# Performance work log

Hardware: AMD Instinct MI355X
Metric: run time of the kernel (lower is better)

Reference implementation:

```python
import jax, jax.numpy as jnp
import numpy as np

N, E, F_IN, HID, HEADS, L, G = 20000, 200000, 20, 128, 4, 4, 32
NEG_SLOPE = 0.2


def setup_inputs() -> dict:
    key = jax.random.key(0)
    ks = jax.random.split(key, 12)
    s = 0.05
    x = jax.random.normal(ks[0], (N, F_IN), jnp.float32)
    edge_index = jax.random.randint(ks[1], (2, E), 0, N, jnp.int32)
    batch = jnp.sort(jax.random.randint(ks[2], (N,), 0, G, jnp.int32))
    W_in = jax.random.normal(ks[3], (F_IN, HID), jnp.float32) * s
    b_in = jnp.zeros((HID,), jnp.float32)
    gat_W = jax.random.normal(ks[4], (L, HID, HEADS * HID), jnp.float32) * s
    att_src = jax.random.normal(ks[5], (L, HEADS, HID), jnp.float32) * s
    att_dst = jax.random.normal(ks[6], (L, HEADS, HID), jnp.float32) * s
    gat_b = jnp.zeros((L, HID), jnp.float32)
    W1 = jax.random.normal(ks[7], (HID, HID // 2), jnp.float32) * s
    b1 = jnp.zeros((HID // 2,), jnp.float32)
    W2 = jax.random.normal(ks[8], (HID // 2, 64), jnp.float32) * s
    b2 = jnp.zeros((64,), jnp.float32)
    W3 = jax.random.normal(ks[9], (64, 32), jnp.float32) * s
    b3 = jnp.zeros((32,), jnp.float32)
    return dict(x=x, edge_index=edge_index, batch=batch, W_in=W_in, b_in=b_in,
                gat_W=gat_W, att_src=att_src, att_dst=att_dst, gat_b=gat_b,
                W1=W1, b1=b1, W2=W2, b2=b2, W3=W3, b3=b3)


def _gat_layer(x, src, dst, W, a_src, a_dst, b):
    # x: [N, HID]; W: [HID, HEADS*HID]; a_*: [HEADS, HID]
    xl = (x @ W).reshape(N, HEADS, HID)                      # [N, H, C]
    al_src = jnp.einsum('nhc,hc->nh', xl, a_src)             # [N, H]
    al_dst = jnp.einsum('nhc,hc->nh', xl, a_dst)             # [N, H]
    e = jax.nn.leaky_relu(al_src[src] + al_dst[dst], NEG_SLOPE)  # [Etot, H]
    # segment softmax over incoming edges of each dst node
    m = jax.ops.segment_max(e, dst, num_segments=N)          # [N, H]
    e = jnp.exp(e - m[dst])
    z = jax.ops.segment_sum(e, dst, num_segments=N)          # [N, H]
    alpha = e / (z[dst] + 1e-16)                             # [Etot, H]
    msg = xl[src] * alpha[:, :, None]                        # [Etot, H, C]
    out = jax.ops.segment_sum(msg, dst, num_segments=N)      # [N, H, C]
    return out.mean(axis=1) + b                              # concat=False: mean over heads


def reference(x, edge_index, batch, W_in, b_in, gat_W, att_src, att_dst, gat_b,
              W1, b1, W2, b2, W3, b3):
    # add self-loops (PyG GATConv default)
    loops = jnp.arange(N, dtype=edge_index.dtype)
    src = jnp.concatenate([edge_index[0], loops])
    dst = jnp.concatenate([edge_index[1], loops])
    h = jax.nn.relu(x @ W_in + b_in)
    for l in range(L):
        h = jax.nn.relu(_gat_layer(h, src, dst, gat_W[l], att_src[l], att_dst[l], gat_b[l])) + h
    # global mean pool per graph
    sums = jax.ops.segment_sum(h, batch, num_segments=G)     # [G, HID]
    cnt = jax.ops.segment_sum(jnp.ones((N,), h.dtype), batch, num_segments=G)
    g = sums / jnp.maximum(cnt, 1.0)[:, None]
    # output MLP (dropout is identity in eval mode)
    g = jax.nn.relu(g @ W1 + b1)
    g = jax.nn.relu(g @ W2 + b2)
    return g @ W3 + b3                                        # [G, 32]
```

## Files before the change

kernel.cpp:

```cpp
#include <hip/hip_runtime.h>

#define N_NODES 20000
#define N_PAD   20032
#define N_EDGES 200000
#define ETOT    (N_EDGES + N_NODES)
#define F_IN    20
#define HID     128
#define HEADS   4
#define FTOT    (HEADS * HID)
#define LAYERS  4
#define NGRAPH  32
#define NEG_SLOPE 0.2f

typedef __attribute__((ext_vector_type(8))) unsigned short ushortx8;
typedef __attribute__((ext_vector_type(8))) short short8;
typedef __attribute__((ext_vector_type(4))) float f32x4;

static __device__ __forceinline__ unsigned short f2bf(float f) {
    unsigned u = __float_as_uint(f);
    u += 0x7FFFu + ((u >> 16) & 1u);
    return (unsigned short)(u >> 16);
}
static __device__ __forceinline__ float bf2f(unsigned short s) {
    return __uint_as_float(((unsigned)s) << 16);
}


__global__ void k_hist(const int* __restrict__ ei, int* __restrict__ deg) {
    int i = blockIdx.x * blockDim.x + threadIdx.x;
    if (i >= ETOT) return;
    int d = (i < N_EDGES) ? ei[N_EDGES + i] : (i - N_EDGES);
    atomicAdd(&deg[d], 1);
}

__global__ __launch_bounds__(1024) void k_scan(const int* __restrict__ deg, int* __restrict__ off) {
    __shared__ int wsum[16];
    __shared__ int carry_s;
    int tid  = threadIdx.x;
    int lane = tid & 63, wv = tid >> 6;
    if (tid == 0) carry_s = 0;
    __syncthreads();
    for (int base = 0; base < N_NODES; base += 1024) {
        int idx = base + tid;
        int v = (idx < N_NODES) ? deg[idx] : 0;
        int x = v;
        #pragma unroll
        for (int s = 1; s < 64; s <<= 1) {
            int t = __shfl_up(x, s, 64);
            if (lane >= s) x += t;
        }
        if (lane == 63) wsum[wv] = x;
        __syncthreads();
        if (wv == 0) {
            int ws = (lane < 16) ? wsum[lane] : 0;
            #pragma unroll
            for (int s = 1; s < 16; s <<= 1) {
                int t = __shfl_up(ws, s, 64);
                if (lane >= s) ws += t;
            }
            if (lane < 16) wsum[lane] = ws;
        }
        __syncthreads();
        int wprev = (wv == 0) ? 0 : wsum[wv - 1];
        int incl  = carry_s + wprev + x;
        if (idx < N_NODES) off[idx] = incl - v;
        __syncthreads();
        if (tid == 1023) carry_s = incl;
        __syncthreads();
    }
    if (threadIdx.x == 0) off[N_NODES] = carry_s;
}

__global__ void k_scatter(const int* __restrict__ ei, const int* __restrict__ off,
                          int* __restrict__ cur, int* __restrict__ csr_src) {
    int i = blockIdx.x * blockDim.x + threadIdx.x;
    if (i >= ETOT) return;
    int s, d;
    if (i < N_EDGES) { s = ei[i]; d = ei[N_EDGES + i]; }
    else             { s = d = i - N_EDGES; }
    int pos = off[d] + atomicAdd(&cur[d], 1);
    csr_src[pos] = s;
}


__global__ void k_bounds(const int* __restrict__ batch, int* __restrict__ gstart) {
    int i = blockIdx.x * blockDim.x + threadIdx.x;
    if (i >= N_NODES) return;
    int b = batch[i];
    int prev = (i == 0) ? -1 : batch[i - 1];
    for (int g = prev + 1; g <= b; ++g) gstart[g] = i;
    if (i == N_NODES - 1) {
        for (int g = b + 1; g <= NGRAPH; ++g) gstart[g] = N_NODES;
    }
}


__global__ void k_wconv(const float* __restrict__ W, unsigned short* __restrict__ wswz) {
    int o = blockIdx.x * 256 + threadIdx.x;
    if (o >= LAYERS * 32 * 4 * 64 * 8) return;
    int e    = o & 7;
    int lane = (o >> 3) & 63;
    int kc   = (o >> 9) & 3;
    int cg   = (o >> 11) & 31;
    int l    = o >> 16;
    int k    = kc * 32 + (lane >> 4) * 8 + e;
    int col  = cg * 16 + (lane & 15);
    wswz[o] = f2bf(W[((size_t)l * HID + k) * FTOT + col]);
}


__global__ __launch_bounds__(256) void k_inproj(const float* __restrict__ x,
                                                const float* __restrict__ W,
                                                const float* __restrict__ b,
                                                float* __restrict__ h,
                                                unsigned short* __restrict__ hb) {
    __shared__ float xs[2][F_IN];
    int tid = threadIdx.x;
    int node0 = blockIdx.x * 2;
    if (tid < 2 * F_IN) {
        int r = tid / F_IN, k = tid % F_IN;
        int nd = node0 + r;
        xs[r][k] = (nd < N_NODES) ? x[nd * F_IN + k] : 0.f;
    }
    __syncthreads();
    int ln = tid >> 7;
    int c  = tid & 127;
    int node = node0 + ln;
    if (node >= N_NODES) return;
    float s = b[c];
    #pragma unroll
    for (int k = 0; k < F_IN; ++k) s += xs[ln][k] * W[k * HID + c];
    float r = fmaxf(s, 0.f);
    h[(size_t)node * HID + c] = r;
    hb[(size_t)node * HID + c] = f2bf(r);
}


__global__ __launch_bounds__(256) void k_gemm(const unsigned short* __restrict__ hb,
                                              const unsigned short* __restrict__ wswz,
                                              unsigned short* __restrict__ xl) {
    int tid  = threadIdx.x;
    int lane = tid & 63;
    int w    = tid >> 6;
    int r0   = blockIdx.x * 64 + w * 16;
    int cgb  = blockIdx.y * 4;
    int arow = r0 + (lane & 15);
    const short8* ap = (const short8*)(hb + (size_t)arow * HID + (lane >> 4) * 8);
    const short8* bp = (const short8*)wswz;
    short8 a[4];
    #pragma unroll
    for (int kc = 0; kc < 4; ++kc) a[kc] = ap[kc * 4];
    f32x4 acc[4];
    #pragma unroll
    for (int ct = 0; ct < 4; ++ct) {
        f32x4 c = {0.f, 0.f, 0.f, 0.f};
        int cg = cgb + ct;
        #pragma unroll
        for (int kc = 0; kc < 4; ++kc) {
            short8 b = bp[(cg * 4 + kc) * 64 + lane];
            c = __builtin_amdgcn_mfma_f32_16x16x32_bf16(a[kc], b, c, 0, 0, 0);
        }
        acc[ct] = c;
    }
    int orow = r0 + (lane >> 4) * 4;
    int ocol = lane & 15;
    #pragma unroll
    for (int ct = 0; ct < 4; ++ct) {
        int col = (cgb + ct) * 16 + ocol;
        #pragma unroll
        for (int r = 0; r < 4; ++r) {
            int row = orow + r;
            if (row < N_NODES) xl[(size_t)row * FTOT + col] = f2bf(acc[ct][r]);
        }
    }
}


__global__ __launch_bounds__(256) void k_att(const unsigned short* __restrict__ xl,
                                             const float* __restrict__ asrc,
                                             const float* __restrict__ adst,
                                             float* __restrict__ al_s,
                                             float* __restrict__ al_d) {
    int wid  = threadIdx.x >> 6;
    int lane = threadIdx.x & 63;
    int node = blockIdx.x * 4 + wid;
    if (node >= N_NODES) return;
    int base = lane * 8;
    ushortx8 xv = *(const ushortx8*)(xl + (size_t)node * FTOT + base);
    float xf[8];
    #pragma unroll
    for (int j = 0; j < 8; ++j) xf[j] = bf2f(xv[j]);
    const float4* s4 = (const float4*)(asrc + base);
    const float4* d4 = (const float4*)(adst + base);
    float4 s0 = s4[0], s1 = s4[1], dd0 = d4[0], dd1 = d4[1];
    float ps = xf[0]*s0.x + xf[1]*s0.y + xf[2]*s0.z + xf[3]*s0.w
             + xf[4]*s1.x + xf[5]*s1.y + xf[6]*s1.z + xf[7]*s1.w;
    float pd = xf[0]*dd0.x + xf[1]*dd0.y + xf[2]*dd0.z + xf[3]*dd0.w
             + xf[4]*dd1.x + xf[5]*dd1.y + xf[6]*dd1.z + xf[7]*dd1.w;
    #pragma unroll
    for (int m = 1; m < 16; m <<= 1) {
        ps += __shfl_xor(ps, m, 64);
        pd += __shfl_xor(pd, m, 64);
    }
    if ((lane & 15) == 0) {
        int hh = lane >> 4;
        al_s[node * HEADS + hh] = ps;
        al_d[node * HEADS + hh] = pd;
    }
}


__global__ __launch_bounds__(256) void k_agg(const unsigned short* __restrict__ xl,
                                             const float* __restrict__ al_s,
                                             const float* __restrict__ al_d,
                                             const int* __restrict__ csr_off,
                                             const int* __restrict__ csr_src,
                                             const float* __restrict__ bias,
                                             float* __restrict__ h,
                                             unsigned short* __restrict__ hb) {
    int wid  = threadIdx.x >> 6;
    int lane = threadIdx.x & 63;
    int node = blockIdx.x * 4 + wid;
    if (node >= N_NODES) return;
    int hh = lane >> 4;
    int e0 = csr_off[node], e1 = csr_off[node + 1];
    float ald = al_d[node * HEADS + hh];

    float m = -1e30f, z = 0.f;
    for (int e = e0 + (lane & 15); e < e1; e += 16) {
        int s = csr_src[e];
        float ev = al_s[s * HEADS + hh] + ald;
        ev = ev > 0.f ? ev : NEG_SLOPE * ev;
        float mn = fmaxf(m, ev);
        z = z * __expf(m - mn) + __expf(ev - mn);
        m = mn;
    }
    #pragma unroll
    for (int msk = 1; msk < 16; msk <<= 1) {
        float m2 = __shfl_xor(m, msk, 64);
        float z2 = __shfl_xor(z, msk, 64);
        float mn = fmaxf(m, m2);
        z = z * __expf(m - mn) + z2 * __expf(m2 - mn);
        m = mn;
    }
    float zinv = 1.f / (z + 1e-16f);

    float acc[8] = {};
    #pragma unroll 2
    for (int e = e0; e < e1; ++e) {
        int s = csr_src[e];
        float ev = al_s[s * HEADS + hh] + ald;
        ev = ev > 0.f ? ev : NEG_SLOPE * ev;
        float alpha = __expf(ev - m) * zinv;
        ushortx8 v = *(const ushortx8*)(xl + (size_t)s * FTOT + lane * 8);
        #pragma unroll
        for (int j = 0; j < 8; ++j) acc[j] += alpha * bf2f(v[j]);
    }
    #pragma unroll
    for (int j = 0; j < 8; ++j) {
        acc[j] += __shfl_xor(acc[j], 16, 64);
        acc[j] += __shfl_xor(acc[j], 32, 64);
    }
    if (lane < 16) {
        int c = lane * 8;
        float4 hv0 = *(const float4*)(h + (size_t)node * HID + c);
        float4 hv1 = *(const float4*)(h + (size_t)node * HID + c + 4);
        float4 b0 = *(const float4*)(bias + c);
        float4 b1 = *(const float4*)(bias + c + 4);
        float4 o0, o1;
        o0.x = fmaxf(acc[0] * 0.25f + b0.x, 0.f) + hv0.x;
        o0.y = fmaxf(acc[1] * 0.25f + b0.y, 0.f) + hv0.y;
        o0.z = fmaxf(acc[2] * 0.25f + b0.z, 0.f) + hv0.z;
        o0.w = fmaxf(acc[3] * 0.25f + b0.w, 0.f) + hv0.w;
        o1.x = fmaxf(acc[4] * 0.25f + b1.x, 0.f) + hv1.x;
        o1.y = fmaxf(acc[5] * 0.25f + b1.y, 0.f) + hv1.y;
        o1.z = fmaxf(acc[6] * 0.25f + b1.z, 0.f) + hv1.z;
        o1.w = fmaxf(acc[7] * 0.25f + b1.w, 0.f) + hv1.w;
        *(float4*)(h + (size_t)node * HID + c)     = o0;
        *(float4*)(h + (size_t)node * HID + c + 4) = o1;
        ushortx8 hv;
        hv[0] = f2bf(o0.x); hv[1] = f2bf(o0.y); hv[2] = f2bf(o0.z); hv[3] = f2bf(o0.w);
        hv[4] = f2bf(o1.x); hv[5] = f2bf(o1.y); hv[6] = f2bf(o1.z); hv[7] = f2bf(o1.w);
        *(ushortx8*)(hb + (size_t)node * HID + c) = hv;
    }
}


__global__ __launch_bounds__(128) void k_pool(const float* __restrict__ h,
                                              const int* __restrict__ gstart,
                                              float* __restrict__ pooled) {
    int g = blockIdx.y;
    int slice = blockIdx.x;
    int tid = threadIdx.x;
    int start = gstart[g];
    int cnt   = gstart[g + 1] - start;
    int per = (cnt + 31) / 32;
    int r0 = slice * per, r1 = min(r0 + per, cnt);
    if (r0 >= r1) return;
    float s0 = 0.f, s1 = 0.f, s2 = 0.f, s3 = 0.f;
    int r = r0;
    for (; r + 3 < r1; r += 4) {
        s0 += h[(size_t)(start + r)     * HID + tid];
        s1 += h[(size_t)(start + r + 1) * HID + tid];
        s2 += h[(size_t)(start + r + 2) * HID + tid];
        s3 += h[(size_t)(start + r + 3) * HID + tid];
    }
    for (; r < r1; ++r) s0 += h[(size_t)(start + r) * HID + tid];
    atomicAdd(&pooled[g * HID + tid], (s0 + s1) + (s2 + s3));
}

__global__ __launch_bounds__(256) void k_mlp(const float* __restrict__ pooled,
                                             const int* __restrict__ gstart,
                                             const float* __restrict__ W1, const float* __restrict__ b1,
                                             const float* __restrict__ W2, const float* __restrict__ b2,
                                             const float* __restrict__ W3, const float* __restrict__ b3,
                                             float* __restrict__ out) {
    int gr = blockIdx.x;
    __shared__ float g[HID];
    __shared__ float part[4][64];
    __shared__ float t1[64], t2[64];
    int tid = threadIdx.x;
    if (tid < HID) {
        float inv = 1.f / fmaxf((float)(gstart[gr + 1] - gstart[gr]), 1.f);
        g[tid] = pooled[gr * HID + tid] * inv;
    }
    __syncthreads();
    {
        int c = tid & 63, q = tid >> 6;
        float s = 0.f;
        #pragma unroll 8
        for (int k = q * 32; k < q * 32 + 32; ++k) s += g[k] * W1[k * 64 + c];
        part[q][c] = s;
        __syncthreads();
        if (tid < 64) t1[tid] = fmaxf(part[0][tid] + part[1][tid] + part[2][tid] + part[3][tid] + b1[tid], 0.f);
        __syncthreads();
    }
    {
        int c = tid & 63, q = tid >> 6;
        float s = 0.f;
        #pragma unroll 8
        for (int k = q * 16; k < q * 16 + 16; ++k) s += t1[k] * W2[k * 64 + c];
        part[q][c] = s;
        __syncthreads();
        if (tid < 64) t2[tid] = fmaxf(part[0][tid] + part[1][tid] + part[2][tid] + part[3][tid] + b2[tid], 0.f);
        __syncthreads();
    }
    {
        int c = tid & 31, q = tid >> 5;
        float s = 0.f;
        #pragma unroll 8
        for (int k = q * 8; k < q * 8 + 8; ++k) s += t2[k] * W3[k * 32 + c];
        float* pf = &part[0][0];
        pf[q * 32 + c] = s;
        __syncthreads();
        if (tid < 32) {
            float r = b3[tid];
            #pragma unroll
            for (int q2 = 0; q2 < 8; ++q2) r += pf[q2 * 32 + tid];
            out[gr * 32 + tid] = r;
        }
    }
}


extern "C" void kernel_launch(void* const* d_in, const int* in_sizes, int n_in,
                              void* d_out, int out_size, void* d_ws, size_t ws_size,
                              hipStream_t stream) {
    const float* x       = (const float*)d_in[0];
    const int*   ei      = (const int*)d_in[1];
    const int*   batch   = (const int*)d_in[2];
    const float* W_in    = (const float*)d_in[3];
    const float* b_in    = (const float*)d_in[4];
    const float* gat_W   = (const float*)d_in[5];
    const float* att_src = (const float*)d_in[6];
    const float* att_dst = (const float*)d_in[7];
    const float* gat_b   = (const float*)d_in[8];
    const float* W1 = (const float*)d_in[9];
    const float* b1 = (const float*)d_in[10];
    const float* W2 = (const float*)d_in[11];
    const float* b2 = (const float*)d_in[12];
    const float* W3 = (const float*)d_in[13];
    const float* b3 = (const float*)d_in[14];
    float* out = (float*)d_out;

    char* ws = (char*)d_ws;
    size_t o = 0;
    auto alloc = [&](size_t nbytes) -> void* {
        void* p = ws + o;
        o += (nbytes + 255) & ~(size_t)255;
        return p;
    };
    int* deg      = (int*)alloc((size_t)2 * N_NODES * 4);
    int* cur      = deg + N_NODES;
    int* gstart   = (int*)alloc((size_t)(NGRAPH + 1) * 4);
    float* pooled = (float*)alloc((size_t)NGRAPH * HID * 4);
    int* csr_off  = (int*)alloc((size_t)(N_NODES + 1) * 4);
    int* csr_src  = (int*)alloc((size_t)ETOT * 4);
    float* h      = (float*)alloc((size_t)N_NODES * HID * 4);
    unsigned short* hb   = (unsigned short*)alloc((size_t)N_PAD * HID * 2);
    unsigned short* xl   = (unsigned short*)alloc((size_t)N_NODES * FTOT * 2);
    unsigned short* wswz = (unsigned short*)alloc((size_t)LAYERS * HID * FTOT * 2);
    float* al_s   = (float*)alloc((size_t)N_NODES * HEADS * 4);
    float* al_d   = (float*)alloc((size_t)N_NODES * HEADS * 4);

    hipMemsetAsync(deg, 0, (size_t)2 * N_NODES * 4, stream);
    hipMemsetAsync(pooled, 0, (size_t)NGRAPH * HID * 4, stream);

    k_hist<<<(ETOT + 255) / 256, 256, 0, stream>>>(ei, deg);
    k_scan<<<1, 1024, 0, stream>>>(deg, csr_off);
    k_scatter<<<(ETOT + 255) / 256, 256, 0, stream>>>(ei, csr_off, cur, csr_src);
    k_bounds<<<(N_NODES + 255) / 256, 256, 0, stream>>>(batch, gstart);
    k_wconv<<<(LAYERS * 32 * 4 * 64 * 8) / 256, 256, 0, stream>>>(gat_W, wswz);

    k_inproj<<<(N_NODES + 1) / 2, 256, 0, stream>>>(x, W_in, b_in, h, hb);

    for (int l = 0; l < LAYERS; ++l) {
        k_gemm<<<dim3(N_PAD / 64, FTOT / 64), 256, 0, stream>>>(
            hb, wswz + (size_t)l * HID * FTOT, xl);
        k_att<<<(N_NODES + 3) / 4, 256, 0, stream>>>(
            xl, att_src + (size_t)l * HEADS * HID, att_dst + (size_t)l * HEADS * HID, al_s, al_d);
        k_agg<<<(N_NODES + 3) / 4, 256, 0, stream>>>(
            xl, al_s, al_d, csr_off, csr_src, gat_b + (size_t)l * HID, h, hb);
    }

    k_pool<<<dim3(32, NGRAPH), 128, 0, stream>>>(h, gstart, pooled);
    k_mlp<<<NGRAPH, 256, 0, stream>>>(pooled, gstart, W1, b1, W2, b2, W3, b3, out);
}
```

Measured before the change: 378.8 us.

## Fuse attention logits into GEMM epilogue and split aggregation across two waves per node

The GEMM now computes one full head (128 columns) per block and folds the att_src/att_dst dot products into its epilogue with shuffle reductions. This removes the separate k_att kernel and its re-read of xl. The aggregation kernel now gives each node two wavefronts, each covering two heads with 4 columns per lane, and combines them through shared memory. That doubles parallelism for the memory-bound gather but adds a __syncthreads and an LDS exchange. The al values are now computed from the fp32 accumulators rather than from bf16-rounded xl, which slightly changes numerics.

Measured after the change: 403.2 us. 6.4% more time.

```diff
diff --git a/kernel.cpp b/kernel.cpp
--- a/kernel.cpp
+++ b/kernel.cpp
@@ -138,23 +138,27 @@
 
 __global__ __launch_bounds__(256) void k_gemm(const unsigned short* __restrict__ hb,
                                               const unsigned short* __restrict__ wswz,
-                                              unsigned short* __restrict__ xl) {
+                                              const float* __restrict__ asrc,
+                                              const float* __restrict__ adst,
+                                              unsigned short* __restrict__ xl,
+                                              float* __restrict__ al_s,
+                                              float* __restrict__ al_d) {
     int tid  = threadIdx.x;
     int lane = tid & 63;
     int w    = tid >> 6;
     int r0   = blockIdx.x * 64 + w * 16;
-    int cgb  = blockIdx.y * 4;
+    int hd   = blockIdx.y;
     int arow = r0 + (lane & 15);
     const short8* ap = (const short8*)(hb + (size_t)arow * HID + (lane >> 4) * 8);
     const short8* bp = (const short8*)wswz;
     short8 a[4];
     #pragma unroll
     for (int kc = 0; kc < 4; ++kc) a[kc] = ap[kc * 4];
-    f32x4 acc[4];
-    #pragma unroll
-    for (int ct = 0; ct < 4; ++ct) {
+    f32x4 acc[8];
+    #pragma unroll
+    for (int ct = 0; ct < 8; ++ct) {
         f32x4 c = {0.f, 0.f, 0.f, 0.f};
-        int cg = cgb + ct;
+        int cg = hd * 8 + ct;
         #pragma unroll
         for (int kc = 0; kc < 4; ++kc) {
             short8 b = bp[(cg * 4 + kc) * 64 + lane];
@@ -162,50 +166,38 @@
         }
         acc[ct] = c;
     }
+    int ocol = lane & 15;
     int orow = r0 + (lane >> 4) * 4;
-    int ocol = lane & 15;
-    #pragma unroll
-    for (int ct = 0; ct < 4; ++ct) {
-        int col = (cgb + ct) * 16 + ocol;
+    float vs[4] = {}, vd[4] = {};
+    #pragma unroll
+    for (int ct = 0; ct < 8; ++ct) {
+        int colg = hd * 128 + ct * 16 + ocol;
+        float as = asrc[colg], ad = adst[colg];
+        #pragma unroll
+        for (int r = 0; r < 4; ++r) {
+            vs[r] += acc[ct][r] * as;
+            vd[r] += acc[ct][r] * ad;
+            int row = orow + r;
+            if (row < N_NODES) xl[(size_t)row * FTOT + colg] = f2bf(acc[ct][r]);
+        }
+    }
+    #pragma unroll
+    for (int msk = 1; msk < 16; msk <<= 1) {
+        #pragma unroll
+        for (int r = 0; r < 4; ++r) {
+            vs[r] += __shfl_xor(vs[r], msk, 64);
+            vd[r] += __shfl_xor(vd[r], msk, 64);
+        }
+    }
+    if (ocol == 0) {
         #pragma unroll
         for (int r = 0; r < 4; ++r) {
             int row = orow + r;
-            if (row < N_NODES) xl[(size_t)row * FTOT + col] = f2bf(acc[ct][r]);
-        }
-    }
-}
-
-
-__global__ __launch_bounds__(256) void k_att(const unsigned short* __restrict__ xl,
-                                             const float* __restrict__ asrc,
-                                             const float* __restrict__ adst,
-                                             float* __restrict__ al_s,
-                                             float* __restrict__ al_d) {
-    int wid  = threadIdx.x >> 6;
-    int lane = threadIdx.x & 63;
-    int node = blockIdx.x * 4 + wid;
-    if (node >= N_NODES) return;
-    int base = lane * 8;
-    ushortx8 xv = *(const ushortx8*)(xl + (size_t)node * FTOT + base);
-    float xf[8];
-    #pragma unroll
-    for (int j = 0; j < 8; ++j) xf[j] = bf2f(xv[j]);
-    const float4* s4 = (const float4*)(asrc + base);
-    const float4* d4 = (const float4*)(adst + base);
-    float4 s0 = s4[0], s1 = s4[1], dd0 = d4[0], dd1 = d4[1];
-    float ps = xf[0]*s0.x + xf[1]*s0.y + xf[2]*s0.z + xf[3]*s0.w
-             + xf[4]*s1.x + xf[5]*s1.y + xf[6]*s1.z + xf[7]*s1.w;
-    float pd = xf[0]*dd0.x + xf[1]*dd0.y + xf[2]*dd0.z + xf[3]*dd0.w
-             + xf[4]*dd1.x + xf[5]*dd1.y + xf[6]*dd1.z + xf[7]*dd1.w;
-    #pragma unroll
-    for (int m = 1; m < 16; m <<= 1) {
-        ps += __shfl_xor(ps, m, 64);
-        pd += __shfl_xor(pd, m, 64);
-    }
-    if ((lane & 15) == 0) {
-        int hh = lane >> 4;
-        al_s[node * HEADS + hh] = ps;
-        al_d[node * HEADS + hh] = pd;
+            if (row < N_NODES) {
+                al_s[row * HEADS + hd] = vs[r];
+                al_d[row * HEADS + hd] = vd[r];
+            }
+        }
     }
 }
 
@@ -218,16 +210,19 @@
                                              const float* __restrict__ bias,
                                              float* __restrict__ h,
                                              unsigned short* __restrict__ hb) {
-    int wid  = threadIdx.x >> 6;
-    int lane = threadIdx.x & 63;
-    int node = blockIdx.x * 4 + wid;
-    if (node >= N_NODES) return;
-    int hh = lane >> 4;
+    __shared__ float buf[2][HID];
+    int tid   = threadIdx.x;
+    int lane  = tid & 63;
+    int w     = tid >> 6;
+    int nip   = w >> 1;
+    int chalf = w & 1;
+    int node  = blockIdx.x * 2 + nip;
+    int hh    = chalf * 2 + (lane >> 5);
     int e0 = csr_off[node], e1 = csr_off[node + 1];
     float ald = al_d[node * HEADS + hh];
 
     float m = -1e30f, z = 0.f;
-    for (int e = e0 + (lane & 15); e < e1; e += 16) {
+    for (int e = e0 + (lane & 31); e < e1; e += 32) {
         int s = csr_src[e];
         float ev = al_s[s * HEADS + hh] + ald;
         ev = ev > 0.f ? ev : NEG_SLOPE * ev;
@@ -236,7 +231,7 @@
         m = mn;
     }
     #pragma unroll
-    for (int msk = 1; msk < 16; msk <<= 1) {
+    for (int msk = 1; msk < 32; msk <<= 1) {
         float m2 = __shfl_xor(m, msk, 64);
         float z2 = __shfl_xor(z, msk, 64);
         float mn = fmaxf(m, m2);
@@ -245,43 +240,59 @@
     }
     float zinv = 1.f / (z + 1e-16f);
 
-    float acc[8] = {};
-    #pragma unroll 2
-    for (int e = e0; e < e1; ++e) {
-        int s = csr_src[e];
-        float ev = al_s[s * HEADS + hh] + ald;
-        ev = ev > 0.f ? ev : NEG_SLOPE * ev;
-        float alpha = __expf(ev - m) * zinv;
-        ushortx8 v = *(const ushortx8*)(xl + (size_t)s * FTOT + lane * 8);
-        #pragma unroll
-        for (int j = 0; j < 8; ++j) acc[j] += alpha * bf2f(v[j]);
-    }
-    #pragma unroll
-    for (int j = 0; j < 8; ++j) {
-        acc[j] += __shfl_xor(acc[j], 16, 64);
-        acc[j] += __shfl_xor(acc[j], 32, 64);
-    }
-    if (lane < 16) {
-        int c = lane * 8;
-        float4 hv0 = *(const float4*)(h + (size_t)node * HID + c);
-        float4 hv1 = *(const float4*)(h + (size_t)node * HID + c + 4);
-        float4 b0 = *(const float4*)(bias + c);
-        float4 b1 = *(const float4*)(bias + c + 4);
-        float4 o0, o1;
-        o0.x = fmaxf(acc[0] * 0.25f + b0.x, 0.f) + hv0.x;
-        o0.y = fmaxf(acc[1] * 0.25f + b0.y, 0.f) + hv0.y;
-        o0.z = fmaxf(acc[2] * 0.25f + b0.z, 0.f) + hv0.z;
-        o0.w = fmaxf(acc[3] * 0.25f + b0.w, 0.f) + hv0.w;
-        o1.x = fmaxf(acc[4] * 0.25f + b1.x, 0.f) + hv1.x;
-        o1.y = fmaxf(acc[5] * 0.25f + b1.y, 0.f) + hv1.y;
-        o1.z = fmaxf(acc[6] * 0.25f + b1.z, 0.f) + hv1.z;
-        o1.w = fmaxf(acc[7] * 0.25f + b1.w, 0.f) + hv1.w;
-        *(float4*)(h + (size_t)node * HID + c)     = o0;
-        *(float4*)(h + (size_t)node * HID + c + 4) = o1;
-        ushortx8 hv;
-        hv[0] = f2bf(o0.x); hv[1] = f2bf(o0.y); hv[2] = f2bf(o0.z); hv[3] = f2bf(o0.w);
-        hv[4] = f2bf(o1.x); hv[5] = f2bf(o1.y); hv[6] = f2bf(o1.z); hv[7] = f2bf(o1.w);
-        *(ushortx8*)(hb + (size_t)node * HID + c) = hv;
+    float acc0 = 0.f, acc1 = 0.f, acc2 = 0.f, acc3 = 0.f;
+    const unsigned short* xbase = xl + chalf * 256 + lane * 4;
+    int e = e0;
+    for (; e + 1 < e1; e += 2) {
+        int s0 = csr_src[e], s1 = csr_src[e + 1];
+        float ev0 = al_s[s0 * HEADS + hh] + ald;
+        float ev1 = al_s[s1 * HEADS + hh] + ald;
+        ushort4 v0 = *(const ushort4*)(xbase + (size_t)s0 * FTOT);
+        ushort4 v1 = *(const ushort4*)(xbase + (size_t)s1 * FTOT);
+        ev0 = ev0 > 0.f ? ev0 : NEG_SLOPE * ev0;
+        ev1 = ev1 > 0.f ? ev1 : NEG_SLOPE * ev1;
+        float a0 = __expf(ev0 - m) * zinv;
+        float a1 = __expf(ev1 - m) * zinv;
+        acc0 += a0 * bf2f(v0.x) + a1 * bf2f(v1.x);
+        acc1 += a0 * bf2f(v0.y) + a1 * bf2f(v1.y);
+        acc2 += a0 * bf2f(v0.z) + a1 * bf2f(v1.z);
+        acc3 += a0 * bf2f(v0.w) + a1 * bf2f(v1.w);
+    }
+    if (e < e1) {
+        int s0 = csr_src[e];
+        float ev0 = al_s[s0 * HEADS + hh] + ald;
+        ushort4 v0 = *(const ushort4*)(xbase + (size_t)s0 * FTOT);
+        ev0 = ev0 > 0.f ? ev0 : NEG_SLOPE * ev0;
+        float a0 = __expf(ev0 - m) * zinv;
+        acc0 += a0 * bf2f(v0.x);
+        acc1 += a0 * bf2f(v0.y);
+        acc2 += a0 * bf2f(v0.z);
+        acc3 += a0 * bf2f(v0.w);
+    }
+    acc0 += __shfl_xor(acc0, 32, 64);
+    acc1 += __shfl_xor(acc1, 32, 64);
+    acc2 += __shfl_xor(acc2, 32, 64);
+    acc3 += __shfl_xor(acc3, 32, 64);
+    if (chalf == 1 && lane < 32) {
+        int c = lane * 4;
+        buf[nip][c]     = acc0;
+        buf[nip][c + 1] = acc1;
+        buf[nip][c + 2] = acc2;
+        buf[nip][c + 3] = acc3;
+    }
+    __syncthreads();
+    if (chalf == 0 && lane < 32) {
+        int c = lane * 4;
+        float4 hv = *(const float4*)(h + (size_t)node * HID + c);
+        float4 bb = *(const float4*)(bias + c);
+        float o0 = fmaxf((acc0 + buf[nip][c])     * 0.25f + bb.x, 0.f) + hv.x;
+        float o1 = fmaxf((acc1 + buf[nip][c + 1]) * 0.25f + bb.y, 0.f) + hv.y;
+        float o2 = fmaxf((acc2 + buf[nip][c + 2]) * 0.25f + bb.z, 0.f) + hv.z;
+        float o3 = fmaxf((acc3 + buf[nip][c + 3]) * 0.25f + bb.w, 0.f) + hv.w;
+        *(float4*)(h + (size_t)node * HID + c) = make_float4(o0, o1, o2, o3);
+        ushort4 hv16;
+        hv16.x = f2bf(o0); hv16.y = f2bf(o1); hv16.z = f2bf(o2); hv16.w = f2bf(o3);
+        *(ushort4*)(hb + (size_t)node * HID + c) = hv16;
     }
 }
 
@@ -415,11 +426,11 @@
     k_inproj<<<(N_NODES + 1) / 2, 256, 0, stream>>>(x, W_in, b_in, h, hb);
 
     for (int l = 0; l < LAYERS; ++l) {
-        k_gemm<<<dim3(N_PAD / 64, FTOT / 64), 256, 0, stream>>>(
-            hb, wswz + (size_t)l * HID * FTOT, xl);
-        k_att<<<(N_NODES + 3) / 4, 256, 0, stream>>>(
-            xl, att_src + (size_t)l * HEADS * HID, att_dst + (size_t)l * HEADS * HID, al_s, al_d);
-        k_agg<<<(N_NODES + 3) / 4, 256, 0, stream>>>(
+        k_gemm<<<dim3(N_PAD / 64, HEADS), 256, 0, stream>>>(
+            hb, wswz + (size_t)l * HID * FTOT,
+            att_src + (size_t)l * HEADS * HID, att_dst + (size_t)l * HEADS * HID,
+            xl, al_s, al_d);
+        k_agg<<<N_NODES / 2, 256, 0, stream>>>(
             xl, al_s, al_d, csr_off, csr_src, gat_b + (size_t)l * HID, h, hb);
     }
 
```
